# Performance work log

Measured on AMD Instinct MI355X. Metric: run time of the kernel, lower is better.

The kernel has to match this reference:

```python
import jax, jax.numpy as jnp
import numpy as np

N, E, B = 100000, 800000, 64
IN, HC1, HC2, NC, SA = 256, 128, 32, 2, 350
NEG = 0.2  # GATv2Conv default negative_slope


def forward(s_x, s_edge_index, s_batch, s_root_n_id,
            Wq, bq, Wk, bk, Wv, bv,
            Wl1, bl1, Wr1, br1, att1, bias1,
            Wl2, bl2, Wr2, br2, att2, bias2,
            Wl3, bl3, Wr3, br3, att3, bias3,
            c1w, c1b, c2W, c2b, c3W, c3b,
            linW, linb, aW1, ab1, aW2, mW1, mb1, mW2, mb2):
    src, dst = s_edge_index[0], s_edge_index[1]
    x_info = s_x
    # --- SelfAttention over seq_len=1 (x.unsqueeze(1)) ---
    z = s_x[:, None, :]                                   # [N,1,IN]
    q = z @ Wq + bq; k = z @ Wk + bk; v = z @ Wv + bv      # [N,1,SA]
    scores = jnp.einsum('nqd,nkd->nqk', q, k) / jnp.sqrt(jnp.float32(SA))
    probs = jax.nn.softmax(scores, axis=-1)
    h = jnp.einsum('nqk,nkd->nqd', probs, v)[:, 0, :]      # [N,SA]

    def gatv2(x, Wl, bl, Wr, br, att, bias):
        # PyG GATv2Conv, heads=1, eval mode (dropout off)
        xl = x @ Wl + bl                                   # source transform [N,O]
        xr = x @ Wr + br                                   # target transform [N,O]
        e = jax.nn.leaky_relu(xl[src] + xr[dst], NEG)      # [E,O]
        s = e @ att                                        # [E]
        smax = jax.ops.segment_max(s, dst, num_segments=N)
        smax = jnp.where(jnp.isfinite(smax), smax, 0.0)
        ex = jnp.exp(s - smax[dst])
        den = jax.ops.segment_sum(ex, dst, num_segments=N)
        alpha = ex / jnp.maximum(den[dst], 1e-16)
        return jax.ops.segment_sum(alpha[:, None] * xl[src], dst, num_segments=N) + bias

    h = jax.nn.relu(gatv2(h, Wl1, bl1, Wr1, br1, att1, bias1))
    h = jax.nn.relu(gatv2(h, Wl2, bl2, Wr2, br2, att2, bias2))
    h = jax.nn.relu(gatv2(h, Wl3, bl3, Wr3, br3, att3, bias3))   # [N,HC2]

    # --- readout: root node feature ++ global mean pool ---
    cnt = jax.ops.segment_sum(jnp.ones((N,), h.dtype), s_batch, num_segments=B)
    pooled = jax.ops.segment_sum(h, s_batch, num_segments=B) / jnp.maximum(cnt, 1.0)[:, None]
    sx = jnp.concatenate([h[s_root_n_id], pooled], axis=-1)       # [B,2*HC2]

    # --- info branch on raw root features ---
    info = x_info[s_root_n_id]                                    # [B,IN]
    info = c1w[0] * info[:, :-2] + c1w[1] * info[:, 1:-1] + c1w[2] * info[:, 2:] + c1b  # Conv1d(1,1,3)
    t = info.T                                                    # [IN-2,B]
    t = jax.nn.relu(c2W @ t + c2b[:, None])                       # [HC1,B]
    t = jax.nn.relu(c3W @ t + c3b[:, None])                       # [HC1//2,B]
    t = t.T                                                       # [B,HC1//2]
    L = t.shape[1]
    t = jax.nn.relu(t.reshape(B, HC2, L // HC2).mean(-1))         # AdaptiveAvgPool1d(HC2)

    sx = jax.nn.relu(sx @ linW + linb)                            # [B,HC2]

    # --- semantic attention over the two views ---
    emb = jnp.stack([sx, t], axis=1)                              # [B,2,HC2]
    w = jnp.tanh(emb @ aW1 + ab1) @ aW2                           # [B,2,1]
    beta = jax.nn.softmax(w, axis=1)
    emb = (beta * emb).sum(1)                                     # [B,HC2]

    return jax.nn.softmax(jnp.tanh(emb @ mW1 + mb1) @ mW2 + mb2, axis=1)  # [B,NC]


def setup_inputs() -> dict:
    keys = iter(jax.random.split(jax.random.key(0), 64))
    def nrm(*shape):
        return jax.random.normal(next(keys), shape, dtype=jnp.float32) * 0.05
    inp = {}
    inp['s_x'] = jax.random.normal(next(keys), (N, IN), dtype=jnp.float32)
    inp['s_edge_index'] = jax.random.randint(next(keys), (2, E), 0, N)
    inp['s_batch'] = jnp.sort(jax.random.randint(next(keys), (N,), 0, B))
    inp['s_root_n_id'] = jax.random.randint(next(keys), (B,), 0, N)
    inp['Wq'] = nrm(IN, SA); inp['bq'] = nrm(SA)
    inp['Wk'] = nrm(IN, SA); inp['bk'] = nrm(SA)
    inp['Wv'] = nrm(IN, SA); inp['bv'] = nrm(SA)
    inp['Wl1'] = nrm(SA, HC1); inp['bl1'] = nrm(HC1)
    inp['Wr1'] = nrm(SA, HC1); inp['br1'] = nrm(HC1)
    inp['att1'] = nrm(HC1); inp['bias1'] = nrm(HC1)
    inp['Wl2'] = nrm(HC1, HC1 // 2); inp['bl2'] = nrm(HC1 // 2)
    inp['Wr2'] = nrm(HC1, HC1 // 2); inp['br2'] = nrm(HC1 // 2)
    inp['att2'] = nrm(HC1 // 2); inp['bias2'] = nrm(HC1 // 2)
    inp['Wl3'] = nrm(HC1 // 2, HC2); inp['bl3'] = nrm(HC2)
    inp['Wr3'] = nrm(HC1 // 2, HC2); inp['br3'] = nrm(HC2)
    inp['att3'] = nrm(HC2); inp['bias3'] = nrm(HC2)
    inp['c1w'] = nrm(3); inp['c1b'] = nrm(1)
    inp['c2W'] = nrm(HC1, IN - 2); inp['c2b'] = nrm(HC1)
    inp['c3W'] = nrm(HC1 // 2, HC1); inp['c3b'] = nrm(HC1 // 2)
    inp['linW'] = nrm(2 * HC2, HC2); inp['linb'] = nrm(HC2)
    inp['aW1'] = nrm(HC2, 16); inp['ab1'] = nrm(16); inp['aW2'] = nrm(16, 1)
    inp['mW1'] = nrm(HC2, 16); inp['mb1'] = nrm(16)
    inp['mW2'] = nrm(16, NC); inp['mb2'] = nrm(NC)
    return inp


def reference(s_x, s_edge_index, s_batch, s_root_n_id,
              Wq, bq, Wk, bk, Wv, bv,
              Wl1, bl1, Wr1, br1, att1, bias1,
              Wl2, bl2, Wr2, br2, att2, bias2,
              Wl3, bl3, Wr3, br3, att3, bias3,
              c1w, c1b, c2W, c2b, c3W, c3b,
              linW, linb, aW1, ab1, aW2, mW1, mb1, mW2, mb2):
    return forward(s_x, s_edge_index, s_batch, s_root_n_id,
                   Wq, bq, Wk, bk, Wv, bv,
                   Wl1, bl1, Wr1, br1, att1, bias1,
                   Wl2, bl2, Wr2, br2, att2, bias2,
                   Wl3, bl3, Wr3, br3, att3, bias3,
                   c1w, c1b, c2W, c2b, c3W, c3b,
                   linW, linb, aW1, ab1, aW2, mW1, mb1, mW2, mb2)
```

## Files before the change

### kernel.cpp

```cpp
#include <hip/hip_runtime.h>
#include <hip/hip_bf16.h>
#include <math.h>

typedef unsigned short ushort_t;
typedef __attribute__((ext_vector_type(8))) short bfrag;
typedef __attribute__((ext_vector_type(4))) float ffrag;

constexpr int N_NODES = 100000;
constexpr int N_EDGES = 800000;
constexpr int NB      = 64;
constexpr int IN_F    = 256;
constexpr int HC1C    = 128;
constexpr int HC2C    = 32;
constexpr int SA_D    = 350;
constexpr float NEG   = 0.2f;

constexpr int SCAN_NBLK = (N_NODES + 255) / 256;
constexpr int MB128     = (N_NODES + 127) / 128;

constexpr size_t OFF_WT1    = 0;
constexpr size_t OFF_WT2    = OFF_WT1 + 65536;
constexpr size_t OFF_WT3    = OFF_WT2 + 16384;
constexpr size_t OFF_BC1    = OFF_WT3 + 4096;
constexpr size_t OFF_BC2    = OFF_BC1 + 256;
constexpr size_t OFF_BC3    = OFF_BC2 + 128;
constexpr size_t OFF_XLR    = OFF_BC3 + 64;
constexpr size_t OFF_H      = OFF_XLR + (size_t)N_NODES * 256;
constexpr size_t OFF_DEG    = OFF_H + (size_t)N_NODES * 128;
constexpr size_t OFF_ROWPTR = OFF_DEG + N_NODES;
constexpr size_t OFF_CURSOR = OFF_ROWPTR + N_NODES + 1;
constexpr size_t OFF_BLKS   = OFF_CURSOR + N_NODES;
constexpr size_t OFF_BLKO   = OFF_BLKS + 512;
constexpr size_t OFF_CSRSRC = OFF_BLKO + 512;
constexpr size_t OFF_POOLED = OFF_CSRSRC + N_EDGES;
constexpr size_t OFF_CNT    = OFF_POOLED + NB * HC2C;
constexpr size_t OFF_SX     = OFF_CNT + NB;
constexpr size_t OFF_INFO   = OFF_SX + NB * HC2C;
constexpr size_t OFF_T1     = OFF_INFO + (size_t)NB * (IN_F - 2);
constexpr size_t OFF_T2     = OFF_T1 + (size_t)HC1C * NB;
constexpr size_t OFF_TT     = OFF_T2 + (size_t)NB * NB;
constexpr size_t WS_FLOATS  = OFF_TT + NB * HC2C;

__device__ __forceinline__ ushort_t f2bf(float f) {
  union { float f; unsigned int u; } a;
  a.f = f;
  unsigned int r = a.u + 0x7FFFu + ((a.u >> 16) & 1u);
  return (ushort_t)(r >> 16);
}
__device__ __forceinline__ float bf2f(ushort_t h) {
  union { unsigned int u; float f; } a;
  a.u = ((unsigned int)h) << 16;
  return a.f;
}
__device__ __forceinline__ float2 bfp(unsigned int u) {
  float2 r;
  r.x = __uint_as_float(u << 16);
  r.y = __uint_as_float(u & 0xFFFF0000u);
  return r;
}
__device__ __forceinline__ void split2(float a, float b, unsigned int& hi, unsigned int& lo) {
  unsigned int ua = __float_as_uint(a), ub = __float_as_uint(b);
  float la = a - __uint_as_float(ua & 0xFFFF0000u);
  float lb = b - __uint_as_float(ub & 0xFFFF0000u);
  hi = __builtin_amdgcn_perm(ub, ua, 0x07060302u);
  lo = __builtin_amdgcn_perm(__float_as_uint(lb), __float_as_uint(la), 0x07060302u);
}

__global__ void k_wcomb(const float* __restrict__ Wv, const float* __restrict__ Wl1,
                        const float* __restrict__ Wr1, ushort_t* __restrict__ WT) {
  int t = blockIdx.x * blockDim.x + threadIdx.x;
  if (t >= 256 * 256) return;
  int n = t & 255;
  int k = t >> 8;
  const float* Wx = (n < 128) ? Wl1 : Wr1;
  int j = n & 127;
  float a = 0.f;
  for (int kk = 0; kk < SA_D; ++kk) a += Wv[k * SA_D + kk] * Wx[kk * 128 + j];
  ushort_t h = f2bf(a);
  WT[(size_t)n * 256 + k] = h;
  WT[65536 + (size_t)n * 256 + k] = f2bf(a - bf2f(h));
}

__global__ void k_bcomb(const float* __restrict__ bv, const float* __restrict__ Wl1,
                        const float* __restrict__ bl1, const float* __restrict__ Wr1,
                        const float* __restrict__ br1, float* __restrict__ bc) {
  int n = threadIdx.x;
  if (n >= 256) return;
  const float* Wx = (n < 128) ? Wl1 : Wr1;
  const float* bx = (n < 128) ? bl1 : br1;
  int j = n & 127;
  float a = bx[j];
  for (int kk = 0; kk < SA_D; ++kk) a += bv[kk] * Wx[kk * 128 + j];
  bc[n] = a;
}

template <int K, int C>
__global__ void k_wpack(const float* __restrict__ Wl, const float* __restrict__ bl,
                        const float* __restrict__ Wr, const float* __restrict__ br,
                        ushort_t* __restrict__ WT, float* __restrict__ bc) {
  constexpr int NN = 2 * C;
  int t = blockIdx.x * blockDim.x + threadIdx.x;
  if (t < NN) bc[t] = (t < C) ? bl[t] : br[t - C];
  if (t >= NN * K) return;
  int n = t % NN;
  int k = t / NN;
  float v = (n < C) ? Wl[k * C + n] : Wr[k * C + (n - C)];
  ushort_t h = f2bf(v);
  WT[(size_t)n * K + k] = h;
  WT[(size_t)NN * K + (size_t)n * K + k] = f2bf(v - bf2f(h));
}

__global__ void k_hist(const int* __restrict__ dst, int* __restrict__ deg) {
  int e = blockIdx.x * blockDim.x + threadIdx.x;
  if (e < N_EDGES) atomicAdd(deg + dst[e], 1);
}

__global__ void k_scan_local(const int* __restrict__ deg, int* __restrict__ row_ptr,
                             int* __restrict__ blk_sum) {
  __shared__ int sh[256];
  int t = threadIdx.x;
  int i = blockIdx.x * 256 + t;
  int v = (i < N_NODES) ? deg[i] : 0;
  sh[t] = v;
  __syncthreads();
  for (int off = 1; off < 256; off <<= 1) {
    int add = (t >= off) ? sh[t - off] : 0;
    __syncthreads();
    sh[t] += add;
    __syncthreads();
  }
  if (i < N_NODES) row_ptr[i] = sh[t] - v;
  if (t == 255) blk_sum[blockIdx.x] = sh[255];
}

__global__ void k_scan_blk(const int* __restrict__ blk_sum, int* __restrict__ blk_off) {
  __shared__ int sh[512];
  int t = threadIdx.x;
  int v = (t < SCAN_NBLK) ? blk_sum[t] : 0;
  sh[t] = v;
  __syncthreads();
  for (int off = 1; off < 512; off <<= 1) {
    int add = (t >= off) ? sh[t - off] : 0;
    __syncthreads();
    sh[t] += add;
    __syncthreads();
  }
  blk_off[t] = sh[t] - v;
}

__global__ void k_scan_add(int* __restrict__ row_ptr, const int* __restrict__ blk_off,
                           int* __restrict__ cursor) {
  int i = blockIdx.x * blockDim.x + threadIdx.x;
  if (i < N_NODES) {
    int v = row_ptr[i] + blk_off[i >> 8];
    row_ptr[i] = v;
    cursor[i] = v;
  }
  if (i == 0) row_ptr[N_NODES] = N_EDGES;
}

__global__ void k_fill(const int* __restrict__ src, const int* __restrict__ dst,
                       int* __restrict__ cursor, int* __restrict__ csr_src) {
  int e = blockIdx.x * blockDim.x + threadIdx.x;
  if (e >= N_EDGES) return;
  int pos = atomicAdd(cursor + dst[e], 1);
  csr_src[pos] = src[e];
}

template <int K, int NN, int BN>
__global__ __launch_bounds__(256) void k_gemm_mfma(const float* __restrict__ x,
                                                   const ushort_t* __restrict__ WT,
                                                   const float* __restrict__ bc,
                                                   ushort_t* __restrict__ out, int M) {
  constexpr int BM  = 128;
  constexpr int BK  = 32;
  constexpr int LDA = BK + 8;
  constexpr int RT  = 4;
  constexpr int CT  = BN / 32;
  __shared__ ushort_t As[2][BM * LDA];
  __shared__ ushort_t Bs[2][BN * LDA];
  const int tid  = threadIdx.x;
  const int wave = tid >> 6;
  const int wrow = wave >> 1;
  const int wcol = wave & 1;
  const int lane = tid & 63;
  const int quad = lane >> 4;
  const int l16  = lane & 15;
  const int m0   = blockIdx.x * BM;
  const int n0   = blockIdx.y * BN;

  ffrag acc[RT][CT];
#pragma unroll
  for (int rt = 0; rt < RT; ++rt)
#pragma unroll
    for (int ct = 0; ct < CT; ++ct) acc[rt][ct] = ffrag{0.f, 0.f, 0.f, 0.f};

  for (int k0 = 0; k0 < K; k0 += BK) {
    __syncthreads();
    {
      int row = tid >> 1;
      int ks  = (tid & 1) * 16;
      int gm  = m0 + row;
      if (gm >= M) gm = M - 1;
      const float4* sp = (const float4*)(x + (size_t)gm * K + k0 + ks);
      float4 f0 = sp[0], f1 = sp[1], f2 = sp[2], f3 = sp[3];
      unsigned int hi[8], lo[8];
      split2(f0.x, f0.y, hi[0], lo[0]);
      split2(f0.z, f0.w, hi[1], lo[1]);
      split2(f1.x, f1.y, hi[2], lo[2]);
      split2(f1.z, f1.w, hi[3], lo[3]);
      split2(f2.x, f2.y, hi[4], lo[4]);
      split2(f2.z, f2.w, hi[5], lo[5]);
      split2(f3.x, f3.y, hi[6], lo[6]);
      split2(f3.z, f3.w, hi[7], lo[7]);
      *(uint4*)&As[0][row * LDA + ks]     = *(uint4*)&hi[0];
      *(uint4*)&As[0][row * LDA + ks + 8] = *(uint4*)&hi[4];
      *(uint4*)&As[1][row * LDA + ks]     = *(uint4*)&lo[0];
      *(uint4*)&As[1][row * LDA + ks + 8] = *(uint4*)&lo[4];
    }
#pragma unroll
    for (int i = tid; i < BN * 4; i += 256) {
      int n  = i >> 2;
      int ks = (i & 3) * 8;
      const ushort_t* gh = WT + (size_t)(n0 + n) * K + k0 + ks;
      *(bfrag*)&Bs[0][n * LDA + ks] = *(const bfrag*)gh;
      *(bfrag*)&Bs[1][n * LDA + ks] = *(const bfrag*)(gh + (size_t)NN * K);
    }
    __syncthreads();

    bfrag a_hi[RT], a_lo[RT];
#pragma unroll
    for (int rt = 0; rt < RT; ++rt) {
      int r = wrow * 64 + rt * 16 + l16;
      a_hi[rt] = *(const bfrag*)&As[0][r * LDA + quad * 8];
      a_lo[rt] = *(const bfrag*)&As[1][r * LDA + quad * 8];
    }
#pragma unroll
    for (int ct = 0; ct < CT; ++ct) {
      int bn = wcol * (BN / 2) + ct * 16 + l16;
      bfrag b_hi = *(const bfrag*)&Bs[0][bn * LDA + quad * 8];
      bfrag b_lo = *(const bfrag*)&Bs[1][bn * LDA + quad * 8];
#pragma unroll
      for (int rt = 0; rt < RT; ++rt) {
        acc[rt][ct] = __builtin_amdgcn_mfma_f32_16x16x32_bf16(a_hi[rt], b_hi, acc[rt][ct], 0, 0, 0);
        acc[rt][ct] = __builtin_amdgcn_mfma_f32_16x16x32_bf16(a_hi[rt], b_lo, acc[rt][ct], 0, 0, 0);
        acc[rt][ct] = __builtin_amdgcn_mfma_f32_16x16x32_bf16(a_lo[rt], b_hi, acc[rt][ct], 0, 0, 0);
      }
    }
  }

#pragma unroll
  for (int rt = 0; rt < RT; ++rt)
#pragma unroll
    for (int ct = 0; ct < CT; ++ct) {
      int n = n0 + wcol * (BN / 2) + ct * 16 + l16;
      float b = bc[n];
#pragma unroll
      for (int r = 0; r < 4; ++r) {
        int m = m0 + wrow * 64 + rt * 16 + quad * 4 + r;
        if (m < M) out[(size_t)m * NN + n] = f2bf(acc[rt][ct][r] + b);
      }
    }
}

template <int C>
__global__ void k_gat(const ushort_t* __restrict__ xlr, const int* __restrict__ row_ptr,
                      const int* __restrict__ csr_src, const float* __restrict__ att,
                      const float* __restrict__ bias, float* __restrict__ h) {
  constexpr int G = C / 8;
  constexpr int RS = 2 * C;
  int t = blockIdx.x * blockDim.x + threadIdx.x;
  int d = t / G;
  int lane = t - d * G;
  if (d >= N_NODES) return;
  float xr[8], a[8];
  {
    uint4 u = *(const uint4*)(xlr + (size_t)d * RS + C + lane * 8);
    float2 p0 = bfp(u.x), p1 = bfp(u.y), p2 = bfp(u.z), p3 = bfp(u.w);
    xr[0] = p0.x; xr[1] = p0.y; xr[2] = p1.x; xr[3] = p1.y;
    xr[4] = p2.x; xr[5] = p2.y; xr[6] = p3.x; xr[7] = p3.y;
  }
  *(float4*)&a[0] = *(const float4*)(att + lane * 8);
  *(float4*)&a[4] = *(const float4*)(att + lane * 8 + 4);
  float acc[8];
#pragma unroll
  for (int j = 0; j < 8; ++j) acc[j] = 0.f;
  float den = 0.f;
  const int e0 = row_ptr[d], e1 = row_ptr[d + 1];
  for (int i = e0; i < e1; ++i) {
    int s = csr_src[i];
    uint4 u = *(const uint4*)(xlr + (size_t)s * RS + lane * 8);
    float xl[8];
    {
      float2 p0 = bfp(u.x), p1 = bfp(u.y), p2 = bfp(u.z), p3 = bfp(u.w);
      xl[0] = p0.x; xl[1] = p0.y; xl[2] = p1.x; xl[3] = p1.y;
      xl[4] = p2.x; xl[5] = p2.y; xl[6] = p3.x; xl[7] = p3.y;
    }
    float p = 0.f;
#pragma unroll
    for (int j = 0; j < 8; ++j) {
      float v = xl[j] + xr[j];
      v = v > 0.f ? v : NEG * v;
      p += a[j] * v;
    }
#pragma unroll
    for (int off = G / 2; off > 0; off >>= 1) p += __shfl_xor(p, off, 64);
    float ex = expf(p);
    den += ex;
#pragma unroll
    for (int j = 0; j < 8; ++j) acc[j] += ex * xl[j];
  }
  float inv = 1.f / fmaxf(den, 1e-16f);
  float o[8];
#pragma unroll
  for (int j = 0; j < 8; ++j)
    o[j] = fmaxf(acc[j] * inv + bias[lane * 8 + j], 0.f);
  float* hp = h + (size_t)d * C + lane * 8;
  *(float4*)hp       = *(float4*)&o[0];
  *(float4*)(hp + 4) = *(float4*)&o[4];
}

__global__ void k_pool(const float* __restrict__ h3, const int* __restrict__ batch,
                       float* __restrict__ pooled, float* __restrict__ cnt) {
  constexpr int NPB = 1024;
  constexpr int NPT = NPB / 8;
  int c = threadIdx.x & 31;
  int r = threadIdx.x >> 5;
  int base = blockIdx.x * NPB + r * NPT;
  if (base >= N_NODES) return;
  int end = base + NPT;
  if (end > N_NODES) end = N_NODES;
  int cur_b = batch[base];
  float acc = 0.f, count = 0.f;
  for (int n = base; n < end; ++n) {
    int b = batch[n];
    if (b != cur_b) {
      atomicAdd(pooled + cur_b * HC2C + c, acc);
      if (c == 0) atomicAdd(cnt + cur_b, count);
      cur_b = b;
      acc = 0.f;
      count = 0.f;
    }
    acc += h3[(size_t)n * HC2C + c];
    count += 1.f;
  }
  atomicAdd(pooled + cur_b * HC2C + c, acc);
  if (c == 0) atomicAdd(cnt + cur_b, count);
}

__global__ void k_sx(const float* __restrict__ h3, const int* __restrict__ root,
                     const float* __restrict__ pooled, const float* __restrict__ cnt,
                     const float* __restrict__ linW, const float* __restrict__ linb,
                     float* __restrict__ sx) {
  int t = blockIdx.x * blockDim.x + threadIdx.x;
  if (t >= NB * HC2C) return;
  int b = t >> 5, j = t & 31;
  int r = root[b];
  float inv = 1.f / fmaxf(cnt[b], 1.0f);
  float a = linb[j];
  for (int c = 0; c < HC2C; ++c) a += h3[(size_t)r * HC2C + c] * linW[c * HC2C + j];
  for (int c = 0; c < HC2C; ++c) a += (pooled[b * HC2C + c] * inv) * linW[(HC2C + c) * HC2C + j];
  sx[t] = a > 0.f ? a : 0.f;
}

__global__ void k_info1(const float* __restrict__ X, const int* __restrict__ root,
                        const float* __restrict__ c1w, const float* __restrict__ c1b,
                        float* __restrict__ info) {
  constexpr int L = IN_F - 2;
  int t = blockIdx.x * blockDim.x + threadIdx.x;
  if (t >= NB * L) return;
  int b = t / L, i = t - (t / L) * L;
  const float* xr = X + (size_t)root[b] * IN_F;
  info[t] = c1w[0] * xr[i] + c1w[1] * xr[i + 1] + c1w[2] * xr[i + 2] + c1b[0];
}

__global__ void k_info2(const float* __restrict__ info, const float* __restrict__ c2W,
                        const float* __restrict__ c2b, float* __restrict__ t1) {
  constexpr int L = IN_F - 2;
  int t = blockIdx.x * blockDim.x + threadIdx.x;
  if (t >= HC1C * NB) return;
  int j = t >> 6, b = t & 63;
  float a = c2b[j];
  for (int i = 0; i < L; ++i) a += c2W[j * L + i] * info[b * L + i];
  t1[t] = a > 0.f ? a : 0.f;
}

__global__ void k_info3(const float* __restrict__ t1, const float* __restrict__ c3W,
                        const float* __restrict__ c3b, float* __restrict__ t2) {
  int t = blockIdx.x * blockDim.x + threadIdx.x;
  if (t >= NB * NB) return;
  int j = t >> 6, b = t & 63;
  float a = c3b[j];
  for (int i = 0; i < HC1C; ++i) a += c3W[j * HC1C + i] * t1[i * NB + b];
  t2[t] = a > 0.f ? a : 0.f;
}

__global__ void k_info4(const float* __restrict__ t2, float* __restrict__ tt) {
  int t = blockIdx.x * blockDim.x + threadIdx.x;
  if (t >= NB * HC2C) return;
  int b = t >> 5, c = t & 31;
  float v = 0.5f * (t2[(2 * c) * NB + b] + t2[(2 * c + 1) * NB + b]);
  tt[b * HC2C + c] = v > 0.f ? v : 0.f;
}

__global__ void k_final(const float* __restrict__ sx, const float* __restrict__ tt,
                        const float* __restrict__ aW1, const float* __restrict__ ab1,
                        const float* __restrict__ aW2, const float* __restrict__ mW1,
                        const float* __restrict__ mb1, const float* __restrict__ mW2,
                        const float* __restrict__ mb2, float* __restrict__ out) {
  int b = threadIdx.x;
  if (b >= NB) return;
  const float* e0 = sx + b * HC2C;
  const float* e1 = tt + b * HC2C;
  float w[2];
#pragma unroll
  for (int r = 0; r < 2; ++r) {
    const float* eb = (r == 0) ? e0 : e1;
    float acc = 0.f;
    for (int j = 0; j < 16; ++j) {
      float z = ab1[j];
      for (int c = 0; c < HC2C; ++c) z += eb[c] * aW1[c * 16 + j];
      acc += tanhf(z) * aW2[j];
    }
    w[r] = acc;
  }
  float mx = fmaxf(w[0], w[1]);
  float x0 = expf(w[0] - mx), x1 = expf(w[1] - mx);
  float inv = 1.f / (x0 + x1);
  float b0 = x0 * inv, b1 = x1 * inv;
  float t16[16];
  for (int j = 0; j < 16; ++j) {
    float z = mb1[j];
    for (int c = 0; c < HC2C; ++c) z += (b0 * e0[c] + b1 * e1[c]) * mW1[c * 16 + j];
    t16[j] = tanhf(z);
  }
  float l0 = mb2[0], l1 = mb2[1];
  for (int j = 0; j < 16; ++j) {
    l0 += t16[j] * mW2[j * 2 + 0];
    l1 += t16[j] * mW2[j * 2 + 1];
  }
  float m2 = fmaxf(l0, l1);
  float y0 = expf(l0 - m2), y1 = expf(l1 - m2);
  float is = 1.f / (y0 + y1);
  out[b * 2 + 0] = y0 * is;
  out[b * 2 + 1] = y1 * is;
}

extern "C" void kernel_launch(void* const* d_in, const int* in_sizes, int n_in, void* d_out,
                              int out_size, void* d_ws, size_t ws_size, hipStream_t stream) {
  if (ws_size < WS_FLOATS * sizeof(float)) return;

  const float* s_x   = (const float*)d_in[0];
  const int*   edge  = (const int*)d_in[1];
  const int*   batch = (const int*)d_in[2];
  const int*   root  = (const int*)d_in[3];
  const float* Wv    = (const float*)d_in[8];
  const float* bv    = (const float*)d_in[9];
  const float* Wl1   = (const float*)d_in[10];
  const float* bl1   = (const float*)d_in[11];
  const float* Wr1   = (const float*)d_in[12];
  const float* br1   = (const float*)d_in[13];
  const float* att1  = (const float*)d_in[14];
  const float* bias1 = (const float*)d_in[15];
  const float* Wl2   = (const float*)d_in[16];
  const float* bl2   = (const float*)d_in[17];
  const float* Wr2   = (const float*)d_in[18];
  const float* br2   = (const float*)d_in[19];
  const float* att2  = (const float*)d_in[20];
  const float* bias2 = (const float*)d_in[21];
  const float* Wl3   = (const float*)d_in[22];
  const float* bl3   = (const float*)d_in[23];
  const float* Wr3   = (const float*)d_in[24];
  const float* br3   = (const float*)d_in[25];
  const float* att3  = (const float*)d_in[26];
  const float* bias3 = (const float*)d_in[27];
  const float* c1w   = (const float*)d_in[28];
  const float* c1b   = (const float*)d_in[29];
  const float* c2W   = (const float*)d_in[30];
  const float* c2b   = (const float*)d_in[31];
  const float* c3W   = (const float*)d_in[32];
  const float* c3b   = (const float*)d_in[33];
  const float* linW  = (const float*)d_in[34];
  const float* linb  = (const float*)d_in[35];
  const float* aW1   = (const float*)d_in[36];
  const float* ab1   = (const float*)d_in[37];
  const float* aW2   = (const float*)d_in[38];
  const float* mW1   = (const float*)d_in[39];
  const float* mb1   = (const float*)d_in[40];
  const float* mW2   = (const float*)d_in[41];
  const float* mb2   = (const float*)d_in[42];

  const int* src = edge;
  const int* dst = edge + N_EDGES;

  float*    ws      = (float*)d_ws;
  ushort_t* WT1     = (ushort_t*)(ws + OFF_WT1);
  ushort_t* WT2     = (ushort_t*)(ws + OFF_WT2);
  ushort_t* WT3     = (ushort_t*)(ws + OFF_WT3);
  float*    bc1     = ws + OFF_BC1;
  float*    bc2     = ws + OFF_BC2;
  float*    bc3     = ws + OFF_BC3;
  ushort_t* xlr     = (ushort_t*)(ws + OFF_XLR);
  float*    hbuf    = ws + OFF_H;
  int*      deg     = (int*)(ws + OFF_DEG);
  int*      row_ptr = (int*)(ws + OFF_ROWPTR);
  int*      cursor  = (int*)(ws + OFF_CURSOR);
  int*      blks    = (int*)(ws + OFF_BLKS);
  int*      blko    = (int*)(ws + OFF_BLKO);
  int*      csr_src = (int*)(ws + OFF_CSRSRC);
  float*    pooled  = ws + OFF_POOLED;
  float*    cnt     = ws + OFF_CNT;
  float*    sx      = ws + OFF_SX;
  float*    info    = ws + OFF_INFO;
  float*    t1      = ws + OFF_T1;
  float*    t2      = ws + OFF_T2;
  float*    tt      = ws + OFF_TT;
  float*    out     = (float*)d_out;

  hipMemsetAsync(deg, 0, N_NODES * sizeof(int), stream);
  k_hist<<<(N_EDGES + 255) / 256, 256, 0, stream>>>(dst, deg);
  k_scan_local<<<SCAN_NBLK, 256, 0, stream>>>(deg, row_ptr, blks);
  k_scan_blk<<<1, 512, 0, stream>>>(blks, blko);
  k_scan_add<<<SCAN_NBLK, 256, 0, stream>>>(row_ptr, blko, cursor);
  k_fill<<<(N_EDGES + 255) / 256, 256, 0, stream>>>(src, dst, cursor, csr_src);

  k_wcomb<<<(256 * 256) / 256, 256, 0, stream>>>(Wv, Wl1, Wr1, WT1);
  k_bcomb<<<1, 256, 0, stream>>>(bv, Wl1, bl1, Wr1, br1, bc1);
  k_wpack<128, 64><<<(128 * 128 + 255) / 256, 256, 0, stream>>>(Wl2, bl2, Wr2, br2, WT2, bc2);
  k_wpack<64, 32><<<(64 * 64 + 255) / 256, 256, 0, stream>>>(Wl3, bl3, Wr3, br3, WT3, bc3);

  k_gemm_mfma<256, 256, 128><<<dim3(MB128, 2), 256, 0, stream>>>(s_x, WT1, bc1, xlr, N_NODES);
  k_gat<128><<<(N_NODES * 16 + 255) / 256, 256, 0, stream>>>(xlr, row_ptr, csr_src, att1,
                                                             bias1, hbuf);

  k_gemm_mfma<128, 128, 128><<<dim3(MB128, 1), 256, 0, stream>>>(hbuf, WT2, bc2, xlr, N_NODES);
  k_gat<64><<<(N_NODES * 8 + 255) / 256, 256, 0, stream>>>(xlr, row_ptr, csr_src, att2,
                                                           bias2, hbuf);

  k_gemm_mfma<64, 64, 64><<<dim3(MB128, 1), 256, 0, stream>>>(hbuf, WT3, bc3, xlr, N_NODES);
  k_gat<32><<<(N_NODES * 4 + 255) / 256, 256, 0, stream>>>(xlr, row_ptr, csr_src, att3,
                                                           bias3, hbuf);

  hipMemsetAsync(pooled, 0, (NB * HC2C + NB) * sizeof(float), stream);
  k_pool<<<(N_NODES + 1023) / 1024, 256, 0, stream>>>(hbuf, batch, pooled, cnt);
  k_sx<<<(NB * HC2C + 255) / 256, 256, 0, stream>>>(hbuf, root, pooled, cnt, linW, linb, sx);

  k_info1<<<(NB * (IN_F - 2) + 255) / 256, 256, 0, stream>>>(s_x, root, c1w, c1b, info);
  k_info2<<<(HC1C * NB + 255) / 256, 256, 0, stream>>>(info, c2W, c2b, t1);
  k_info3<<<(NB * NB + 255) / 256, 256, 0, stream>>>(t1, c3W, c3b, t2);
  k_info4<<<(NB * HC2C + 255) / 256, 256, 0, stream>>>(t2, tt);

  k_final<<<1, NB, 0, stream>>>(sx, tt, aW1, ab1, aW2, mW1, mb1, mW2, mb2, out);
}
```

Baseline: 689.1 us.

## Drop split-bf16 GEMM compensation, store hidden activations as bf16, double-buffer tiles

Replaces the three-MFMA hi/lo split-bf16 GEMM with a single plain bf16 MFMA per tile and packs weights as single bf16. GAT outputs are written as bf16, which halves activation traffic, and the next GEMM consumes them directly without conversion. The GEMM also gains register-staged double buffering so global loads overlap with MFMA work. In exchange it gives up the near-fp32 accuracy of the split scheme, so errors may grow against the reference tolerance.

```diff
diff --git a/kernel.cpp b/kernel.cpp
--- a/kernel.cpp
+++ b/kernel.cpp
@@ -58,12 +58,12 @@
   r.y = __uint_as_float(u & 0xFFFF0000u);
   return r;
 }
-__device__ __forceinline__ void split2(float a, float b, unsigned int& hi, unsigned int& lo) {
-  unsigned int ua = __float_as_uint(a), ub = __float_as_uint(b);
-  float la = a - __uint_as_float(ua & 0xFFFF0000u);
-  float lb = b - __uint_as_float(ub & 0xFFFF0000u);
-  hi = __builtin_amdgcn_perm(ub, ua, 0x07060302u);
-  lo = __builtin_amdgcn_perm(__float_as_uint(lb), __float_as_uint(la), 0x07060302u);
+__device__ __forceinline__ unsigned int pack2(float a, float b) {
+  unsigned int ua = __float_as_uint(a);
+  ua += 0x7FFFu + ((ua >> 16) & 1u);
+  unsigned int ub = __float_as_uint(b);
+  ub += 0x7FFFu + ((ub >> 16) & 1u);
+  return __builtin_amdgcn_perm(ub, ua, 0x07060302u);
 }
 
 __global__ void k_wcomb(const float* __restrict__ Wv, const float* __restrict__ Wl1,
@@ -76,9 +76,7 @@
   int j = n & 127;
   float a = 0.f;
   for (int kk = 0; kk < SA_D; ++kk) a += Wv[k * SA_D + kk] * Wx[kk * 128 + j];
-  ushort_t h = f2bf(a);
-  WT[(size_t)n * 256 + k] = h;
-  WT[65536 + (size_t)n * 256 + k] = f2bf(a - bf2f(h));
+  WT[(size_t)n * 256 + k] = f2bf(a);
 }
 
 __global__ void k_bcomb(const float* __restrict__ bv, const float* __restrict__ Wl1,
@@ -105,9 +103,7 @@
   int n = t % NN;
   int k = t / NN;
   float v = (n < C) ? Wl[k * C + n] : Wr[k * C + (n - C)];
-  ushort_t h = f2bf(v);
-  WT[(size_t)n * K + k] = h;
-  WT[(size_t)NN * K + (size_t)n * K + k] = f2bf(v - bf2f(h));
+  WT[(size_t)n * K + k] = f2bf(v);
 }
 
 __global__ void k_hist(const int* __restrict__ dst, int* __restrict__ deg) {
@@ -167,16 +163,18 @@
   csr_src[pos] = src[e];
 }
 
-template <int K, int NN, int BN>
-__global__ __launch_bounds__(256) void k_gemm_mfma(const float* __restrict__ x,
+template <int K, int NN, int BN, bool AF32>
+__global__ __launch_bounds__(256) void k_gemm_bf16(const void* __restrict__ xin,
                                                    const ushort_t* __restrict__ WT,
                                                    const float* __restrict__ bc,
                                                    ushort_t* __restrict__ out, int M) {
-  constexpr int BM  = 128;
-  constexpr int BK  = 32;
-  constexpr int LDA = BK + 8;
-  constexpr int RT  = 4;
-  constexpr int CT  = BN / 32;
+  constexpr int BM    = 128;
+  constexpr int BK    = 32;
+  constexpr int LDA   = BK + 8;
+  constexpr int RT    = 4;
+  constexpr int CT    = BN / 32;
+  constexpr int NSTEP = K / BK;
+  constexpr int NBCH  = (BN * 4) / 256;
   __shared__ ushort_t As[2][BM * LDA];
   __shared__ ushort_t Bs[2][BN * LDA];
   const int tid  = threadIdx.x;
@@ -189,64 +187,80 @@
   const int m0   = blockIdx.x * BM;
   const int n0   = blockIdx.y * BN;
 
+  const int arow = tid >> 1;
+  const int aks  = (tid & 1) * 16;
+  int gm = m0 + arow;
+  if (gm >= M) gm = M - 1;
+
+  float4 fA[4];
+  uint4  uA[2];
+  uint4  uB[NBCH];
+
+  auto loadT = [&](int k0) {
+    if (AF32) {
+      const float4* sp = (const float4*)((const float*)xin + (size_t)gm * K + k0 + aks);
+      fA[0] = sp[0]; fA[1] = sp[1]; fA[2] = sp[2]; fA[3] = sp[3];
+    } else {
+      const uint4* sp = (const uint4*)((const ushort_t*)xin + (size_t)gm * K + k0 + aks);
+      uA[0] = sp[0]; uA[1] = sp[1];
+    }
+#pragma unroll
+    for (int c = 0; c < NBCH; ++c) {
+      int ch = tid + c * 256;
+      int n  = ch >> 2;
+      int ks = (ch & 3) * 8;
+      uB[c] = *(const uint4*)(WT + (size_t)(n0 + n) * K + k0 + ks);
+    }
+  };
+  auto storeT = [&](int buf) {
+    if (AF32) {
+      uint4 p0, p1;
+      p0.x = pack2(fA[0].x, fA[0].y); p0.y = pack2(fA[0].z, fA[0].w);
+      p0.z = pack2(fA[1].x, fA[1].y); p0.w = pack2(fA[1].z, fA[1].w);
+      p1.x = pack2(fA[2].x, fA[2].y); p1.y = pack2(fA[2].z, fA[2].w);
+      p1.z = pack2(fA[3].x, fA[3].y); p1.w = pack2(fA[3].z, fA[3].w);
+      *(uint4*)&As[buf][arow * LDA + aks]     = p0;
+      *(uint4*)&As[buf][arow * LDA + aks + 8] = p1;
+    } else {
+      *(uint4*)&As[buf][arow * LDA + aks]     = uA[0];
+      *(uint4*)&As[buf][arow * LDA + aks + 8] = uA[1];
+    }
+#pragma unroll
+    for (int c = 0; c < NBCH; ++c) {
+      int ch = tid + c * 256;
+      int n  = ch >> 2;
+      int ks = (ch & 3) * 8;
+      *(uint4*)&Bs[buf][n * LDA + ks] = uB[c];
+    }
+  };
+
   ffrag acc[RT][CT];
 #pragma unroll
   for (int rt = 0; rt < RT; ++rt)
 #pragma unroll
     for (int ct = 0; ct < CT; ++ct) acc[rt][ct] = ffrag{0.f, 0.f, 0.f, 0.f};
 
-  for (int k0 = 0; k0 < K; k0 += BK) {
+  loadT(0);
+  storeT(0);
+  __syncthreads();
+
+  for (int i = 0; i < NSTEP; ++i) {
+    const int cur = i & 1;
+    if (i + 1 < NSTEP) loadT((i + 1) * BK);
+    bfrag a[RT], b[CT];
+#pragma unroll
+    for (int rt = 0; rt < RT; ++rt)
+      a[rt] = *(const bfrag*)&As[cur][(wrow * 64 + rt * 16 + l16) * LDA + quad * 8];
+#pragma unroll
+    for (int ct = 0; ct < CT; ++ct)
+      b[ct] = *(const bfrag*)&Bs[cur][(wcol * (BN / 2) + ct * 16 + l16) * LDA + quad * 8];
+#pragma unroll
+    for (int ct = 0; ct < CT; ++ct)
+#pragma unroll
+      for (int rt = 0; rt < RT; ++rt)
+        acc[rt][ct] = __builtin_amdgcn_mfma_f32_16x16x32_bf16(a[rt], b[ct], acc[rt][ct], 0, 0, 0);
+    if (i + 1 < NSTEP) storeT(1 - cur);
     __syncthreads();
-    {
-      int row = tid >> 1;
-      int ks  = (tid & 1) * 16;
-      int gm  = m0 + row;
-      if (gm >= M) gm = M - 1;
-      const float4* sp = (const float4*)(x + (size_t)gm * K + k0 + ks);
-      float4 f0 = sp[0], f1 = sp[1], f2 = sp[2], f3 = sp[3];
-      unsigned int hi[8], lo[8];
-      split2(f0.x, f0.y, hi[0], lo[0]);
-      split2(f0.z, f0.w, hi[1], lo[1]);
-      split2(f1.x, f1.y, hi[2], lo[2]);
-      split2(f1.z, f1.w, hi[3], lo[3]);
-      split2(f2.x, f2.y, hi[4], lo[4]);
-      split2(f2.z, f2.w, hi[5], lo[5]);
-      split2(f3.x, f3.y, hi[6], lo[6]);
-      split2(f3.z, f3.w, hi[7], lo[7]);
-      *(uint4*)&As[0][row * LDA + ks]     = *(uint4*)&hi[0];
-      *(uint4*)&As[0][row * LDA + ks + 8] = *(uint4*)&hi[4];
-      *(uint4*)&As[1][row * LDA + ks]     = *(uint4*)&lo[0];
-      *(uint4*)&As[1][row * LDA + ks + 8] = *(uint4*)&lo[4];
-    }
-#pragma unroll
-    for (int i = tid; i < BN * 4; i += 256) {
-      int n  = i >> 2;
-      int ks = (i & 3) * 8;
-      const ushort_t* gh = WT + (size_t)(n0 + n) * K + k0 + ks;
-      *(bfrag*)&Bs[0][n * LDA + ks] = *(const bfrag*)gh;
-      *(bfrag*)&Bs[1][n * LDA + ks] = *(const bfrag*)(gh + (size_t)NN * K);
-    }
-    __syncthreads();
-
-    bfrag a_hi[RT], a_lo[RT];
-#pragma unroll
-    for (int rt = 0; rt < RT; ++rt) {
-      int r = wrow * 64 + rt * 16 + l16;
-      a_hi[rt] = *(const bfrag*)&As[0][r * LDA + quad * 8];
-      a_lo[rt] = *(const bfrag*)&As[1][r * LDA + quad * 8];
-    }
-#pragma unroll
-    for (int ct = 0; ct < CT; ++ct) {
-      int bn = wcol * (BN / 2) + ct * 16 + l16;
-      bfrag b_hi = *(const bfrag*)&Bs[0][bn * LDA + quad * 8];
-      bfrag b_lo = *(const bfrag*)&Bs[1][bn * LDA + quad * 8];
-#pragma unroll
-      for (int rt = 0; rt < RT; ++rt) {
-        acc[rt][ct] = __builtin_amdgcn_mfma_f32_16x16x32_bf16(a_hi[rt], b_hi, acc[rt][ct], 0, 0, 0);
-        acc[rt][ct] = __builtin_amdgcn_mfma_f32_16x16x32_bf16(a_hi[rt], b_lo, acc[rt][ct], 0, 0, 0);
-        acc[rt][ct] = __builtin_amdgcn_mfma_f32_16x16x32_bf16(a_lo[rt], b_hi, acc[rt][ct], 0, 0, 0);
-      }
-    }
   }
 
 #pragma unroll
@@ -266,7 +280,7 @@
 template <int C>
 __global__ void k_gat(const ushort_t* __restrict__ xlr, const int* __restrict__ row_ptr,
                       const int* __restrict__ csr_src, const float* __restrict__ att,
-                      const float* __restrict__ bias, float* __restrict__ h) {
+                      const float* __restrict__ bias, ushort_t* __restrict__ h) {
   constexpr int G = C / 8;
   constexpr int RS = 2 * C;
   int t = blockIdx.x * blockDim.x + threadIdx.x;
@@ -315,12 +329,15 @@
 #pragma unroll
   for (int j = 0; j < 8; ++j)
     o[j] = fmaxf(acc[j] * inv + bias[lane * 8 + j], 0.f);
-  float* hp = h + (size_t)d * C + lane * 8;
-  *(float4*)hp       = *(float4*)&o[0];
-  *(float4*)(hp + 4) = *(float4*)&o[4];
-}
-
-__global__ void k_pool(const float* __restrict__ h3, const int* __restrict__ batch,
+  uint4 pk;
+  pk.x = pack2(o[0], o[1]);
+  pk.y = pack2(o[2], o[3]);
+  pk.z = pack2(o[4], o[5]);
+  pk.w = pack2(o[6], o[7]);
+  *(uint4*)(h + (size_t)d * C + lane * 8) = pk;
+}
+
+__global__ void k_pool(const ushort_t* __restrict__ h3, const int* __restrict__ batch,
                        float* __restrict__ pooled, float* __restrict__ cnt) {
   constexpr int NPB = 1024;
   constexpr int NPT = NPB / 8;
@@ -341,14 +358,14 @@
       acc = 0.f;
       count = 0.f;
     }
-    acc += h3[(size_t)n * HC2C + c];
+    acc += bf2f(h3[(size_t)n * HC2C + c]);
     count += 1.f;
   }
   atomicAdd(pooled + cur_b * HC2C + c, acc);
   if (c == 0) atomicAdd(cnt + cur_b, count);
 }
 
-__global__ void k_sx(const float* __restrict__ h3, const int* __restrict__ root,
+__global__ void k_sx(const ushort_t* __restrict__ h3, const int* __restrict__ root,
                      const float* __restrict__ pooled, const float* __restrict__ cnt,
                      const float* __restrict__ linW, const float* __restrict__ linb,
                      float* __restrict__ sx) {
@@ -358,7 +375,7 @@
   int r = root[b];
   float inv = 1.f / fmaxf(cnt[b], 1.0f);
   float a = linb[j];
-  for (int c = 0; c < HC2C; ++c) a += h3[(size_t)r * HC2C + c] * linW[c * HC2C + j];
+  for (int c = 0; c < HC2C; ++c) a += bf2f(h3[(size_t)r * HC2C + c]) * linW[c * HC2C + j];
   for (int c = 0; c < HC2C; ++c) a += (pooled[b * HC2C + c] * inv) * linW[(HC2C + c) * HC2C + j];
   sx[t] = a > 0.f ? a : 0.f;
 }
@@ -501,7 +518,7 @@
   float*    bc2     = ws + OFF_BC2;
   float*    bc3     = ws + OFF_BC3;
   ushort_t* xlr     = (ushort_t*)(ws + OFF_XLR);
-  float*    hbuf    = ws + OFF_H;
+  ushort_t* hbuf    = (ushort_t*)(ws + OFF_H);
   int*      deg     = (int*)(ws + OFF_DEG);
   int*      row_ptr = (int*)(ws + OFF_ROWPTR);
   int*      cursor  = (int*)(ws + OFF_CURSOR);
@@ -529,15 +546,18 @@
   k_wpack<128, 64><<<(128 * 128 + 255) / 256, 256, 0, stream>>>(Wl2, bl2, Wr2, br2, WT2, bc2);
   k_wpack<64, 32><<<(64 * 64 + 255) / 256, 256, 0, stream>>>(Wl3, bl3, Wr3, br3, WT3, bc3);
 
-  k_gemm_mfma<256, 256, 128><<<dim3(MB128, 2), 256, 0, stream>>>(s_x, WT1, bc1, xlr, N_NODES);
+  k_gemm_bf16<256, 256, 128, true><<<dim3(MB128, 2), 256, 0, stream>>>(s_x, WT1, bc1, xlr,
+                                                                       N_NODES);
   k_gat<128><<<(N_NODES * 16 + 255) / 256, 256, 0, stream>>>(xlr, row_ptr, csr_src, att1,
                                                              bias1, hbuf);
 
-  k_gemm_mfma<128, 128, 128><<<dim3(MB128, 1), 256, 0, stream>>>(hbuf, WT2, bc2, xlr, N_NODES);
+  k_gemm_bf16<128, 128, 128, false><<<dim3(MB128, 1), 256, 0, stream>>>(hbuf, WT2, bc2, xlr,
+                                                                        N_NODES);
   k_gat<64><<<(N_NODES * 8 + 255) / 256, 256, 0, stream>>>(xlr, row_ptr, csr_src, att2,
                                                            bias2, hbuf);
 
-  k_gemm_mfma<64, 64, 64><<<dim3(MB128, 1), 256, 0, stream>>>(hbuf, WT3, bc3, xlr, N_NODES);
+  k_gemm_bf16<64, 64, 64, false><<<dim3(MB128, 1), 256, 0, stream>>>(hbuf, WT3, bc3, xlr,
+                                                                     N_NODES);
   k_gat<32><<<(N_NODES * 4 + 255) / 256, 256, 0, stream>>>(xlr, row_ptr, csr_src, att3,
                                                            bias3, hbuf);
 
```

New measurement: 680.8 us. About the same (-1.2%).
